# Kernel optimization log

Hardware: AMD Instinct MI355X
Metric: run time of the kernel (lower is better)

Reference implementation:

```python
import jax, jax.numpy as jnp
import numpy as np

EPS = 1e-5

def conv2d(x, w, stride=1, padding=1, dilation=1):
    # x: [N, C, H, W], w: [O, I, kh, kw]
    return jax.lax.conv_general_dilated(
        x, w, (stride, stride), [(padding, padding), (padding, padding)],
        rhs_dilation=(dilation, dilation),
        dimension_numbers=('NCHW', 'OIHW', 'NCHW'))


def setup_inputs() -> dict:
    key = jax.random.key(0)
    ks = jax.random.split(key, 7)
    T, N, Cin, H, W = 16, 4, 64, 64, 64
    Cout = 64
    x = jax.random.normal(ks[0], (T, N, Cin, H, W), dtype=jnp.float32)
    gamma = jnp.ones((Cin,), jnp.float32)
    beta = jnp.zeros((Cin,), jnp.float32)
    conv1_w = jax.random.normal(ks[1], (3 * Cout, Cin, 3, 3), jnp.float32) * 0.02
    conv1_b = jax.random.normal(ks[2], (3 * Cout,), jnp.float32) * 0.02
    w_h2h = jax.random.normal(ks[3], (3 * Cout, Cout, 3, 3), jnp.float32) * 0.02
    w_c2h = jax.random.normal(ks[4], (3 * Cout, Cout, 3, 3), jnp.float32) * 0.02
    return {"x": x, "gamma": gamma, "beta": beta, "conv1_w": conv1_w,
            "conv1_b": conv1_b, "w_h2h": w_h2h, "w_c2h": w_c2h}


def reference(x, gamma, beta, conv1_w, conv1_b, w_h2h, w_c2h):
    T, N, Cin, H, W = x.shape
    Cout = w_h2h.shape[1]
    # time_to_batch: [T, N, C, H, W] -> [T*N, C, H, W]
    xb = x.reshape(T * N, Cin, H, W)
    # BatchNorm2d (training mode: biased batch stats over N*T, H, W)
    mean = jnp.mean(xb, axis=(0, 2, 3), keepdims=True)
    var = jnp.var(xb, axis=(0, 2, 3), keepdims=True)
    g = gamma.reshape(1, Cin, 1, 1)
    b = beta.reshape(1, Cin, 1, 1)
    bnx = (xb - mean) * jax.lax.rsqrt(var + EPS) * g + b
    # conv1: Cin -> 3*Cout
    y = conv2d(bnx, conv1_w, stride=1, padding=1) + conv1_b.reshape(1, -1, 1, 1)
    # batch_to_time: -> [T, N, 3*Cout, H, W]
    y = y.reshape(T, N, 3 * Cout, H, W)

    # ConvLSTMCell: zero init state is exact (h2h/c2h convs have no bias)
    h0 = jnp.zeros((N, Cout, H, W), y.dtype)
    c0 = jnp.zeros((N, Cout, H, W), y.dtype)

    def step(carry, yt):
        h, c = carry
        tmp = conv2d(c, w_c2h, padding=1) + conv2d(h, w_h2h, padding=1) + yt
        cc_f, cc_o, cc_g = jnp.split(tmp, 3, axis=1)
        f = jax.nn.sigmoid(cc_f)
        o = jax.nn.sigmoid(cc_o)
        gg = jnp.tanh(cc_g)
        c_new = f * c + (1.0 - f) * gg
        h_new = o * jnp.tanh(c_new)
        return (h_new, c_new), h_new

    _, hs = jax.lax.scan(step, (h0, c0), y)
    return hs  # [T, N, Cout, H, W]
```

## Files before the change

### kernel.cpp

```cpp
#include <hip/hip_runtime.h>

typedef unsigned short u16;
typedef unsigned int   u32;
typedef __attribute__((ext_vector_type(8))) short short8;
typedef __attribute__((ext_vector_type(4))) float f32x4;

typedef __attribute__((address_space(1))) const void GASV;
typedef __attribute__((address_space(3))) void LASV;

#define IMG_BYTES  557568
#define WS_SCALE   0
#define WS_SHIFT   256
#define WS_PART    512
#define WS_WA      8704
#define WS_BNXP    672256
#define WS_HC      (WS_BNXP + 64*IMG_BYTES)
#define WS_CSTATE  (WS_HC + 16*IMG_BYTES)

#define SM_RING_OFF 38016
#define SMEM_TOT    (38016 + 4*12288)

__device__ __forceinline__ u16 f2b(float f){
  u32 x = __float_as_uint(f);
  return (u16)((x + 0x7fffu + ((x>>16)&1u)) >> 16);
}
__device__ __forceinline__ float sigm(float x){ return 1.f/(1.f+__expf(-x)); }
__device__ __forceinline__ float tanh_(float x){
  float e = __expf(2.f*fabsf(x));
  float t = 1.f - 2.f/(e+1.f);
  return copysignf(t, x);
}

__global__ void k_wt(const float* __restrict__ c1, const float* __restrict__ c2h,
                     const float* __restrict__ h2h, u16* __restrict__ wA){
  int idx = blockIdx.x*256 + threadIdx.x;
  int e = idx & 7;
  int lane = (idx >> 3) & 63;
  int v = idx >> 9;
  int f2 = v % 12;  v /= 12;
  int oh = v & 1;
  int stage = v >> 1;
  int cc = f2 / 6, gate = (f2 % 6) >> 1, og2 = f2 & 1;
  int j = stage / 9, tap = stage % 9;
  int och = gate*64 + (oh*2 + og2)*16 + (lane & 15);
  int c = cc*32 + (lane >> 4)*8 + e;
  const float* src = (j==0) ? c1 : ((j==1) ? c2h : h2h);
  wA[idx] = f2b(src[(och*64 + c)*9 + tap]);
}

__global__ void k_bnsum(const float* __restrict__ x, float* __restrict__ part){
  int c = blockIdx.x & 63, g = blockIdx.x >> 6;
  int tid = threadIdx.x, w = tid >> 6, lane = tid & 63;
  float s = 0.f, s2 = 0.f;
  for (int im = 0; im < 4; ++im){
    const float* base = x + (((size_t)((g*4+im)*64 + c)) << 12);
    #pragma unroll
    for (int it = 0; it < 4; ++it){
      float4 v = *(const float4*)(base + (((it<<8) + tid) << 2));
      s  += v.x + v.y + v.z + v.w;
      s2 += v.x*v.x + v.y*v.y + v.z*v.z + v.w*v.w;
    }
  }
  #pragma unroll
  for (int off = 32; off > 0; off >>= 1){
    s  += __shfl_down(s,  off);
    s2 += __shfl_down(s2, off);
  }
  __shared__ float red[8];
  if (lane == 0){ red[w] = s; red[4+w] = s2; }
  __syncthreads();
  if (tid == 0){
    float S  = red[0]+red[1]+red[2]+red[3];
    float S2 = red[4]+red[5]+red[6]+red[7];
    part[(g<<7) + c] = S;
    part[(g<<7) + 64 + c] = S2;
  }
}

__global__ void k_bnfin(const float* __restrict__ part, const float* __restrict__ gamma,
                        const float* __restrict__ beta, float* __restrict__ scale,
                        float* __restrict__ shift){
  int c = threadIdx.x;
  float S = 0.f, S2 = 0.f;
  for (int g = 0; g < 16; ++g){ S += part[(g<<7)+c]; S2 += part[(g<<7)+64+c]; }
  const float inv = 1.f/262144.f;
  float mean = S*inv;
  float var  = S2*inv - mean*mean;
  float sc = gamma[c] * rsqrtf(var + 1e-5f);
  scale[c] = sc;
  shift[c] = beta[c] - mean*sc;
}

__global__ void k_bnx(const float* __restrict__ x, const float* __restrict__ scale,
                      const float* __restrict__ shift, char* __restrict__ bnxp){
  int img = blockIdx.x / 66, rp = blockIdx.x % 66;
  int tid = threadIdx.x;
  char* dstrow = bnxp + (size_t)img*IMG_BYTES + (size_t)rp*8448;
  const uint4 z = {0,0,0,0};
  if (rp == 0 || rp == 65){
    for (int i = tid; i < 528; i += 256) ((uint4*)dstrow)[i] = z;
    return;
  }
  if (tid < 16)
    *(uint4*)(dstrow + (tid>>3)*(65*128) + (tid&7)*16) = z;
  int r = rp - 1;
  int col = tid & 63, cq = tid >> 6;
  const float* xb = x + (((size_t)(img*64 + cq*16)) << 12) + (r<<6) + col;
  union { u16 u[16]; uint4 v[2]; } pk;
  #pragma unroll
  for (int i = 0; i < 16; ++i){
    int c = cq*16 + i;
    float vv = xb[((size_t)i) << 12];
    pk.u[i] = f2b(vv*scale[c] + shift[c]);
  }
  char* dst = dstrow + (size_t)(col + 1)*128 + cq*32;
  *(uint4*)dst = pk.v[0];
  *(uint4*)(dst+16) = pk.v[1];
}

#define STAGE_W(v) do {                                                         \
  if (w < 4){                                                                   \
    int _vj = jp + (v)/9; if (_vj >= 3) _vj -= 3;                               \
    int _vt = tp + (v)%9; if (_vt >= 9) _vt -= 9;                               \
    const char* _gs = wA + ((size_t)((_vj*9 + _vt)*2 + oh))*12288               \
                        + w*3072 + lane*16;                                     \
    char* _ls = smem + SM_RING_OFF + ((v)&3)*12288 + w*3072;                    \
    __builtin_amdgcn_global_load_lds((GASV*)(_gs),        (LASV*)(_ls),        16, 0, 0); \
    __builtin_amdgcn_global_load_lds((GASV*)(_gs + 1024), (LASV*)(_ls + 1024), 16, 0, 0); \
    __builtin_amdgcn_global_load_lds((GASV*)(_gs + 2048), (LASV*)(_ls + 2048), 16, 0, 0); \
  }                                                                             \
} while(0)

#define WAITN_BAR(N) do {                                                       \
  asm volatile("s_waitcnt vmcnt(" #N ")\n\ts_barrier" ::: "memory");            \
  __builtin_amdgcn_sched_barrier(0);                                            \
} while(0)

__global__ __launch_bounds__(512, 1) void k_step(
    const char* __restrict__ bnxp,
    const char* __restrict__ cpad_s, const char* __restrict__ hpad_s,
    char* __restrict__ cpad_d, char* __restrict__ hpad_d,
    const char* __restrict__ wA, const float* __restrict__ b1,
    float* __restrict__ cstate, float* __restrict__ out, int t)
{
  extern __shared__ __align__(16) char smem[];
  const int tid = threadIdx.x;
  const int w = tid >> 6, lane = tid & 63;
  const int l15 = lane & 15, l4 = lane >> 4;
  const int wr = w >> 2, og2 = (w >> 1) & 1, ch = w & 1;
  const int bid = blockIdx.x;
  const int oh = bid & 1, rp = (bid >> 1) & 31, n = bid >> 6;
  const int jp = bid % 3, tp = bid % 9;

  const char* gb0 = bnxp   + (size_t)(t*4+n)*IMG_BYTES + rp*16896;
  const char* gb1 = cpad_s + (size_t)n*IMG_BYTES + rp*16896;
  const char* gb2 = hpad_s + (size_t)n*IMG_BYTES + rp*16896;

  f32x4 acc[3][2];
  #pragma unroll
  for (int a = 0; a < 3; ++a)
    #pragma unroll
    for (int b = 0; b < 2; ++b)
      acc[a][b] = (f32x4){0.f,0.f,0.f,0.f};

  STAGE_W(0); STAGE_W(1); STAGE_W(2);

  #pragma unroll
  for (int jj = 0; jj < 3; ++jj){
    int jv = jp + jj; if (jv >= 3) jv -= 3;
    const char* gbj = (jv==0) ? gb0 : ((jv==1) ? gb1 : gb2);
    for (int i = tid; i < 2112; i += 512){
      int rr = i / 528, iw = i % 528;
      *(uint4*)(smem + rr*9504 + (iw>>3)*144 + (iw&7)*16) =
          *(const uint4*)(gbj + rr*8448 + iw*16);
    }
    __syncthreads();

    #pragma unroll
    for (int tt = 0; tt < 9; ++tt){
      const int u = jj*9 + tt;
      if (u <= 23) STAGE_W(u+3);
      {
        int tv = tp + tt; if (tv >= 9) tv -= 9;
        const int kh = tv/3, kw = tv - kh*3;
        const char* ab0 = smem + SM_RING_OFF + (u&3)*12288 + og2*1024 + lane*16;
        const char* ib0 = smem + (wr + kh)*9504 + ((ch<<5) + kw + l15)*144 + l4*16;
        #pragma unroll
        for (int cc = 0; cc < 2; ++cc){
          short8 af = *(const short8*)(ab0 + cc*6144);
          short8 ao = *(const short8*)(ab0 + cc*6144 + 2048);
          short8 ag = *(const short8*)(ab0 + cc*6144 + 4096);
          #pragma unroll
          for (int cf = 0; cf < 2; ++cf){
            short8 bf = *(const short8*)(ib0 + cc*64 + cf*2304);
            acc[0][cf] = __builtin_amdgcn_mfma_f32_16x16x32_bf16(af, bf, acc[0][cf], 0,0,0);
            acc[1][cf] = __builtin_amdgcn_mfma_f32_16x16x32_bf16(ao, bf, acc[1][cf], 0,0,0);
            acc[2][cf] = __builtin_amdgcn_mfma_f32_16x16x32_bf16(ag, bf, acc[2][cf], 0,0,0);
          }
        }
      }
      if (u <= 23)      WAITN_BAR(6);
      else if (u == 24) WAITN_BAR(3);
      else if (u == 25) WAITN_BAR(0);
    }
  }

  const int r = (rp << 1) + wr;
  const size_t cb = ((size_t)(n*64)) << 12;
  const size_t ob = ((size_t)((t*4+n)*64)) << 12;
  const int gc0 = ((oh<<1) + og2)*16 + l4*4;
  char* hrow = hpad_d + (size_t)n*IMG_BYTES + (size_t)(r+1)*8448;
  char* crow = cpad_d + (size_t)n*IMG_BYTES + (size_t)(r+1)*8448;

  #pragma unroll
  for (int cf = 0; cf < 2; ++cf){
    const int col = (ch<<5) + (cf<<4) + l15;
    const int p = (r<<6) + col;
    union { u16 u[4]; uint2 v; } hp, cp2;
    #pragma unroll
    for (int reg = 0; reg < 4; ++reg){
      const int gc = gc0 + reg;
      float fv = acc[0][cf][reg] + b1[gc];
      float ov = acc[1][cf][reg] + b1[64+gc];
      float gv = acc[2][cf][reg] + b1[128+gc];
      float f  = sigm(fv);
      float og_ = sigm(ov);
      float g  = tanh_(gv);
      float* cptr = cstate + cb + (((size_t)gc)<<12) + p;
      float cprev = *cptr;
      float cn = f*cprev + (1.f-f)*g;
      float hn = og_ * tanh_(cn);
      *cptr = cn;
      out[ob + (((size_t)gc)<<12) + p] = hn;
      hp.u[reg]  = f2b(hn);
      cp2.u[reg] = f2b(cn);
    }
    *(uint2*)(hrow + (size_t)(col+1)*128 + gc0*2) = hp.v;
    *(uint2*)(crow + (size_t)(col+1)*128 + gc0*2) = cp2.v;
  }
}

extern "C" void kernel_launch(void* const* d_in, const int* in_sizes, int n_in,
                              void* d_out, int out_size, void* d_ws, size_t ws_size,
                              hipStream_t stream)
{
  (void)in_sizes; (void)n_in; (void)out_size; (void)ws_size;
  const float* x     = (const float*)d_in[0];
  const float* gamma = (const float*)d_in[1];
  const float* beta  = (const float*)d_in[2];
  const float* c1w   = (const float*)d_in[3];
  const float* c1b   = (const float*)d_in[4];
  const float* wh2h  = (const float*)d_in[5];
  const float* wc2h  = (const float*)d_in[6];
  char* ws  = (char*)d_ws;
  float* out = (float*)d_out;

  hipFuncSetAttribute(reinterpret_cast<const void*>(k_step),
                      hipFuncAttributeMaxDynamicSharedMemorySize, SMEM_TOT);

  char* hpad0 = ws + WS_HC;
  char* cpad0 = ws + WS_HC + (size_t)4*IMG_BYTES;
  char* hpad1 = ws + WS_HC + (size_t)8*IMG_BYTES;
  char* cpad1 = ws + WS_HC + (size_t)12*IMG_BYTES;

  hipMemsetAsync(ws + WS_HC, 0, (size_t)16*IMG_BYTES, stream);
  hipMemsetAsync(ws + WS_CSTATE, 0, (size_t)4*64*4096*4, stream);

  k_wt<<<1296, 256, 0, stream>>>(c1w, wc2h, wh2h, (u16*)(ws + WS_WA));
  k_bnsum<<<1024, 256, 0, stream>>>(x, (float*)(ws + WS_PART));
  k_bnfin<<<1, 64, 0, stream>>>((const float*)(ws + WS_PART), gamma, beta,
                                (float*)(ws + WS_SCALE), (float*)(ws + WS_SHIFT));
  k_bnx<<<4224, 256, 0, stream>>>(x, (const float*)(ws + WS_SCALE),
                                  (const float*)(ws + WS_SHIFT), ws + WS_BNXP);
  for (int t = 0; t < 16; ++t){
    const char* cs = (t & 1) ? cpad1 : cpad0;
    const char* hs = (t & 1) ? hpad1 : hpad0;
    char* cd = (t & 1) ? cpad0 : cpad1;
    char* hd = (t & 1) ? hpad0 : hpad1;
    k_step<<<256, 512, SMEM_TOT, stream>>>(ws + WS_BNXP, cs, hs, cd, hd,
                                           ws + WS_WA, c1b,
                                           (float*)(ws + WS_CSTATE), out, t);
  }
}
```

Measured before the change: 372.5 us.

## Deepen weight ring to six slots, pair taps per barrier, thread-local cell state

The LDS weight ring grows from four to six slots, so weights are prefetched four taps ahead and two kernel taps are computed between each barrier, halving barrier count. MFMA sections are raised with s_setprio. Cell state now lives in a per-thread contiguous slot read and written as vectors, with the t==0 case zeroed in registers, which removes the memset and the strided fp32 loads and stores. Bias values are hoisted into registers. More LDS is used per block.

```diff
diff --git a/kernel.cpp b/kernel.cpp
--- a/kernel.cpp
+++ b/kernel.cpp
@@ -14,11 +14,11 @@
 #define WS_PART    512
 #define WS_WA      8704
 #define WS_BNXP    672256
-#define WS_HC      (WS_BNXP + 64*IMG_BYTES)
-#define WS_CSTATE  (WS_HC + 16*IMG_BYTES)
+#define WS_HC      (WS_BNXP + (size_t)64*IMG_BYTES)
+#define WS_CSTATE  (WS_HC + (size_t)16*IMG_BYTES)
 
 #define SM_RING_OFF 38016
-#define SMEM_TOT    (38016 + 4*12288)
+#define SMEM_TOT    (38016 + 6*12288)
 
 __device__ __forceinline__ u16 f2b(float f){
   u32 x = __float_as_uint(f);
@@ -70,10 +70,8 @@
   if (lane == 0){ red[w] = s; red[4+w] = s2; }
   __syncthreads();
   if (tid == 0){
-    float S  = red[0]+red[1]+red[2]+red[3];
-    float S2 = red[4]+red[5]+red[6]+red[7];
-    part[(g<<7) + c] = S;
-    part[(g<<7) + 64 + c] = S2;
+    part[(g<<7) + c] = red[0]+red[1]+red[2]+red[3];
+    part[(g<<7) + 64 + c] = red[4]+red[5]+red[6]+red[7];
   }
 }
 
@@ -110,8 +108,7 @@
   #pragma unroll
   for (int i = 0; i < 16; ++i){
     int c = cq*16 + i;
-    float vv = xb[((size_t)i) << 12];
-    pk.u[i] = f2b(vv*scale[c] + shift[c]);
+    pk.u[i] = f2b(xb[((size_t)i) << 12]*scale[c] + shift[c]);
   }
   char* dst = dstrow + (size_t)(col + 1)*128 + cq*32;
   *(uint4*)dst = pk.v[0];
@@ -119,12 +116,12 @@
 }
 
 #define STAGE_W(v) do {                                                         \
-  if (w < 4){                                                                   \
+  if ((v) <= 26 && w < 4){                                                      \
     int _vj = jp + (v)/9; if (_vj >= 3) _vj -= 3;                               \
     int _vt = tp + (v)%9; if (_vt >= 9) _vt -= 9;                               \
     const char* _gs = wA + ((size_t)((_vj*9 + _vt)*2 + oh))*12288               \
                         + w*3072 + lane*16;                                     \
-    char* _ls = smem + SM_RING_OFF + ((v)&3)*12288 + w*3072;                    \
+    char* _ls = smem + SM_RING_OFF + ((v)%6)*12288 + w*3072;                    \
     __builtin_amdgcn_global_load_lds((GASV*)(_gs),        (LASV*)(_ls),        16, 0, 0); \
     __builtin_amdgcn_global_load_lds((GASV*)(_gs + 1024), (LASV*)(_ls + 1024), 16, 0, 0); \
     __builtin_amdgcn_global_load_lds((GASV*)(_gs + 2048), (LASV*)(_ls + 2048), 16, 0, 0); \
@@ -134,6 +131,26 @@
 #define WAITN_BAR(N) do {                                                       \
   asm volatile("s_waitcnt vmcnt(" #N ")\n\ts_barrier" ::: "memory");            \
   __builtin_amdgcn_sched_barrier(0);                                            \
+} while(0)
+
+#define COMPUTE(u) do {                                                         \
+  int tv = tp + (u)%9; if (tv >= 9) tv -= 9;                                    \
+  const int kh = tv/3, kw = tv - kh*3;                                          \
+  const char* ab0 = smem + SM_RING_OFF + ((u)%6)*12288 + og2*1024 + lane*16;    \
+  const char* ib0 = smem + (wr + kh)*9504 + ((ch<<5) + kw + l15)*144 + (l4<<4); \
+  _Pragma("unroll")                                                             \
+  for (int cc = 0; cc < 2; ++cc){                                               \
+    short8 af = *(const short8*)(ab0 + cc*6144);                                \
+    short8 ao = *(const short8*)(ab0 + cc*6144 + 2048);                         \
+    short8 ag = *(const short8*)(ab0 + cc*6144 + 4096);                         \
+    _Pragma("unroll")                                                           \
+    for (int cf = 0; cf < 2; ++cf){                                             \
+      short8 bf = *(const short8*)(ib0 + (cf<<4)*144 + (cc<<6));                \
+      acc[0][cf] = __builtin_amdgcn_mfma_f32_16x16x32_bf16(af, bf, acc[0][cf], 0,0,0); \
+      acc[1][cf] = __builtin_amdgcn_mfma_f32_16x16x32_bf16(ao, bf, acc[1][cf], 0,0,0); \
+      acc[2][cf] = __builtin_amdgcn_mfma_f32_16x16x32_bf16(ag, bf, acc[2][cf], 0,0,0); \
+    }                                                                           \
+  }                                                                             \
 } while(0)
 
 __global__ __launch_bounds__(512, 1) void k_step(
@@ -156,6 +173,27 @@
   const char* gb1 = cpad_s + (size_t)n*IMG_BYTES + rp*16896;
   const char* gb2 = hpad_s + (size_t)n*IMG_BYTES + rp*16896;
 
+  float* cslot = cstate + ((size_t)bid*512 + tid)*8;
+  float cpv[8];
+  if (t == 0){
+    #pragma unroll
+    for (int i = 0; i < 8; ++i) cpv[i] = 0.f;
+  } else {
+    f32x4 c0 = *(const f32x4*)cslot;
+    f32x4 c1v = *(const f32x4*)(cslot + 4);
+    cpv[0]=c0[0]; cpv[1]=c0[1]; cpv[2]=c0[2]; cpv[3]=c0[3];
+    cpv[4]=c1v[0]; cpv[5]=c1v[1]; cpv[6]=c1v[2]; cpv[7]=c1v[3];
+  }
+
+  const int gc0 = ((oh<<1) + og2)*16 + l4*4;
+  float bv[12];
+  #pragma unroll
+  for (int reg = 0; reg < 4; ++reg){
+    bv[reg]   = b1[gc0+reg];
+    bv[4+reg] = b1[64+gc0+reg];
+    bv[8+reg] = b1[128+gc0+reg];
+  }
+
   f32x4 acc[3][2];
   #pragma unroll
   for (int a = 0; a < 3; ++a)
@@ -163,7 +201,7 @@
     for (int b = 0; b < 2; ++b)
       acc[a][b] = (f32x4){0.f,0.f,0.f,0.f};
 
-  STAGE_W(0); STAGE_W(1); STAGE_W(2);
+  STAGE_W(0); STAGE_W(1); STAGE_W(2); STAGE_W(3);
 
   #pragma unroll
   for (int jj = 0; jj < 3; ++jj){
@@ -177,41 +215,32 @@
     __syncthreads();
 
     #pragma unroll
-    for (int tt = 0; tt < 9; ++tt){
-      const int u = jj*9 + tt;
-      if (u <= 23) STAGE_W(u+3);
-      {
-        int tv = tp + tt; if (tv >= 9) tv -= 9;
-        const int kh = tv/3, kw = tv - kh*3;
-        const char* ab0 = smem + SM_RING_OFF + (u&3)*12288 + og2*1024 + lane*16;
-        const char* ib0 = smem + (wr + kh)*9504 + ((ch<<5) + kw + l15)*144 + l4*16;
-        #pragma unroll
-        for (int cc = 0; cc < 2; ++cc){
-          short8 af = *(const short8*)(ab0 + cc*6144);
-          short8 ao = *(const short8*)(ab0 + cc*6144 + 2048);
-          short8 ag = *(const short8*)(ab0 + cc*6144 + 4096);
-          #pragma unroll
-          for (int cf = 0; cf < 2; ++cf){
-            short8 bf = *(const short8*)(ib0 + cc*64 + cf*2304);
-            acc[0][cf] = __builtin_amdgcn_mfma_f32_16x16x32_bf16(af, bf, acc[0][cf], 0,0,0);
-            acc[1][cf] = __builtin_amdgcn_mfma_f32_16x16x32_bf16(ao, bf, acc[1][cf], 0,0,0);
-            acc[2][cf] = __builtin_amdgcn_mfma_f32_16x16x32_bf16(ag, bf, acc[2][cf], 0,0,0);
-          }
-        }
-      }
-      if (u <= 23)      WAITN_BAR(6);
-      else if (u == 24) WAITN_BAR(3);
-      else if (u == 25) WAITN_BAR(0);
+    for (int pp = 0; pp < 4; ++pp){
+      const int u = jj*9 + 2*pp;
+      STAGE_W(u+4); STAGE_W(u+5);
+      __builtin_amdgcn_s_setprio(1);
+      COMPUTE(u);
+      COMPUTE(u+1);
+      __builtin_amdgcn_s_setprio(0);
+      if (u == 22)      WAITN_BAR(3);
+      else if (u == 24) WAITN_BAR(0);
+      else              WAITN_BAR(6);
+    }
+    {
+      const int u = jj*9 + 8;
+      STAGE_W(u+4);
+      __builtin_amdgcn_s_setprio(1);
+      COMPUTE(u);
+      __builtin_amdgcn_s_setprio(0);
     }
   }
 
   const int r = (rp << 1) + wr;
-  const size_t cb = ((size_t)(n*64)) << 12;
   const size_t ob = ((size_t)((t*4+n)*64)) << 12;
-  const int gc0 = ((oh<<1) + og2)*16 + l4*4;
   char* hrow = hpad_d + (size_t)n*IMG_BYTES + (size_t)(r+1)*8448;
   char* crow = cpad_d + (size_t)n*IMG_BYTES + (size_t)(r+1)*8448;
 
+  float cnew[8];
   #pragma unroll
   for (int cf = 0; cf < 2; ++cf){
     const int col = (ch<<5) + (cf<<4) + l15;
@@ -220,17 +249,12 @@
     #pragma unroll
     for (int reg = 0; reg < 4; ++reg){
       const int gc = gc0 + reg;
-      float fv = acc[0][cf][reg] + b1[gc];
-      float ov = acc[1][cf][reg] + b1[64+gc];
-      float gv = acc[2][cf][reg] + b1[128+gc];
-      float f  = sigm(fv);
-      float og_ = sigm(ov);
-      float g  = tanh_(gv);
-      float* cptr = cstate + cb + (((size_t)gc)<<12) + p;
-      float cprev = *cptr;
-      float cn = f*cprev + (1.f-f)*g;
+      float f  = sigm(acc[0][cf][reg] + bv[reg]);
+      float og_ = sigm(acc[1][cf][reg] + bv[4+reg]);
+      float g  = tanh_(acc[2][cf][reg] + bv[8+reg]);
+      float cn = f*cpv[cf*4+reg] + (1.f-f)*g;
       float hn = og_ * tanh_(cn);
-      *cptr = cn;
+      cnew[cf*4+reg] = cn;
       out[ob + (((size_t)gc)<<12) + p] = hn;
       hp.u[reg]  = f2b(hn);
       cp2.u[reg] = f2b(cn);
@@ -238,6 +262,8 @@
     *(uint2*)(hrow + (size_t)(col+1)*128 + gc0*2) = hp.v;
     *(uint2*)(crow + (size_t)(col+1)*128 + gc0*2) = cp2.v;
   }
+  *(f32x4*)cslot       = (f32x4){cnew[0],cnew[1],cnew[2],cnew[3]};
+  *(f32x4*)(cslot + 4) = (f32x4){cnew[4],cnew[5],cnew[6],cnew[7]};
 }
 
 extern "C" void kernel_launch(void* const* d_in, const int* in_sizes, int n_in,
@@ -264,7 +290,6 @@
   char* cpad1 = ws + WS_HC + (size_t)12*IMG_BYTES;
 
   hipMemsetAsync(ws + WS_HC, 0, (size_t)16*IMG_BYTES, stream);
-  hipMemsetAsync(ws + WS_CSTATE, 0, (size_t)4*64*4096*4, stream);
 
   k_wt<<<1296, 256, 0, stream>>>(c1w, wc2h, wh2h, (u16*)(ws + WS_WA));
   k_bnsum<<<1024, 256, 0, stream>>>(x, (float*)(ws + WS_PART));
```

Result: faster. 363.7 us (-2.3%).
